# Kernel tuning notes

Measured on AMD Instinct MI355X. Metric: run time of the kernel, lower is better.

## Reference

```python
import jax, jax.numpy as jnp
import numpy as np

NUM_GRAPHS = 128

def gcn_conv(x, edge_index, W, b):
    # PyG GCNConv: add self-loops, sym-normalize, aggregate.
    n = x.shape[0]
    src, dst = edge_index[0], edge_index[1]
    h = x @ W                                   # [N, H]
    deg = jnp.zeros((n,), h.dtype).at[dst].add(1.0) + 1.0  # +1 for self-loop
    dinv = jax.lax.rsqrt(deg)                   # deg^-1/2
    norm = dinv[src] * dinv[dst]                # [E]
    msg = h[src] * norm[:, None]                # [E, H] gathered messages
    agg = jnp.zeros_like(h).at[dst].add(msg)    # scatter-add to dst
    agg = agg + h * (dinv * dinv)[:, None]      # self-loop term
    return agg + b


def setup_inputs() -> dict:
    key = jax.random.key(0)
    ks = jax.random.split(key, 12)
    N, E, F, H, C = 50000, 800000, 64, 64, 16
    x = jax.random.normal(ks[0], (N, F), jnp.float32)
    edge_index = jax.random.randint(ks[1], (2, E), 0, N, jnp.int64)
    batch = jnp.sort(jax.random.randint(ks[2], (N,), 0, NUM_GRAPHS, jnp.int64))
    s = lambda k, sh: jax.random.normal(k, sh, jnp.float32) * (1.0 / np.sqrt(sh[0]))
    return {
        "x": x, "edge_index": edge_index, "batch": batch,
        "W1": s(ks[3], (F, H)), "b1": jnp.zeros((H,), jnp.float32),
        "W2": s(ks[4], (H, H)), "b2": jnp.zeros((H,), jnp.float32),
        "Wc1": s(ks[5], (H, H)), "bc1": jnp.zeros((H,), jnp.float32),
        "Wc2": s(ks[6], (H, C)), "bc2": jnp.zeros((C,), jnp.float32),
    }


def reference(x, edge_index, batch, W1, b1, W2, b2, Wc1, bc1, Wc2, bc2):
    h = gcn_conv(x, edge_index, W1, b1)
    h = jax.nn.relu(h)
    # F.dropout(p=0.5, training=self.training): identity in eval mode
    h = gcn_conv(h, edge_index, W2, b2)
    # global mean pool over graphs
    sums = jax.ops.segment_sum(h, batch, num_segments=NUM_GRAPHS)
    cnts = jax.ops.segment_sum(jnp.ones((h.shape[0],), h.dtype), batch,
                               num_segments=NUM_GRAPHS)
    graph_reps = sums / jnp.maximum(cnts, 1.0)[:, None]
    logits = jax.nn.relu(graph_reps @ Wc1 + bc1) @ Wc2 + bc2
    return (h, graph_reps, logits)
```

## Files before the change

### kernel.cpp

```cpp
#include <hip/hip_runtime.h>
#include <hip/hip_bf16.h>

typedef __hip_bfloat16 bf16;

#define NGRAPH 128
#define MAXNB 256
#define BCAP 8192

__global__ __launch_bounds__(256) void bucket_count_kernel(const int* __restrict__ ei,
                                                           int* __restrict__ bucket_cnt,
                                                           int E, int N, int nb) {
    __shared__ int hist[MAXNB];
    for (int i = threadIdx.x; i < nb; i += 256) hist[i] = 0;
    __syncthreads();
    int stride = gridDim.x * 256;
    for (int e = blockIdx.x * 256 + threadIdx.x; e < E; e += stride) {
        int d = ei[E + e];
        d = max(0, min(d, N - 1));
        atomicAdd(&hist[d >> 8], 1);
    }
    __syncthreads();
    for (int i = threadIdx.x; i < nb; i += 256) {
        int c = hist[i];
        if (c) atomicAdd(&bucket_cnt[i], c);
    }
}

__global__ __launch_bounds__(256) void bucket_scan_kernel(const int* __restrict__ bucket_cnt,
                                                          int* __restrict__ bucket_off,
                                                          int* __restrict__ bucket_cur, int nb) {
    __shared__ int tmp[256];
    int tid = threadIdx.x;
    int v = (tid < nb) ? bucket_cnt[tid] : 0;
    tmp[tid] = v;
    __syncthreads();
    for (int off = 1; off < 256; off <<= 1) {
        int t = (tid >= off) ? tmp[tid - off] : 0;
        __syncthreads();
        tmp[tid] += t;
        __syncthreads();
    }
    int excl = tmp[tid] - v;
    if (tid < nb) { bucket_off[tid] = excl; bucket_cur[tid] = excl; }
    if (tid == nb - 1) bucket_off[nb] = excl + v;
}

__global__ __launch_bounds__(256) void bucket_scatter_kernel(const int* __restrict__ ei,
                                                             int* __restrict__ bucket_cur,
                                                             int2* __restrict__ pairbuf,
                                                             int E, int N, int nb) {
    __shared__ int hist[MAXNB];
    int nwg = gridDim.x;
    int chunk = (E + nwg - 1) / nwg;
    int e0 = blockIdx.x * chunk;
    int e1 = e0 + chunk; if (e1 > E) e1 = E;
    if (e0 >= e1) return;
    for (int i = threadIdx.x; i < nb; i += 256) hist[i] = 0;
    __syncthreads();
    for (int e = e0 + threadIdx.x; e < e1; e += 256) {
        int d = ei[E + e];
        d = max(0, min(d, N - 1));
        atomicAdd(&hist[d >> 8], 1);
    }
    __syncthreads();
    for (int i = threadIdx.x; i < nb; i += 256) {
        int c = hist[i];
        hist[i] = c ? atomicAdd(&bucket_cur[i], c) : 0;
    }
    __syncthreads();
    for (int e = e0 + threadIdx.x; e < e1; e += 256) {
        int s = ei[e];     s = max(0, min(s, N - 1));
        int d = ei[E + e]; d = max(0, min(d, N - 1));
        int pos = atomicAdd(&hist[d >> 8], 1);
        pairbuf[pos] = make_int2(s, d);
    }
}

__global__ __launch_bounds__(256) void bucket_build_kernel(const int2* __restrict__ pairbuf,
                                                           const int* __restrict__ bucket_off,
                                                           int* __restrict__ row_start,
                                                           float* __restrict__ dinv,
                                                           int* __restrict__ csr_src,
                                                           int E, int N, int nb) {
    __shared__ int deg_l[256];
    __shared__ int cur_l[256];
    __shared__ int stage[BCAP];
    int b = blockIdx.x;
    int node0 = b << 8;
    int nn = N - node0; if (nn > 256) nn = 256;
    int p0 = bucket_off[b], p1 = bucket_off[b + 1];
    int ne = p1 - p0;
    int tid = threadIdx.x;
    deg_l[tid] = 0;
    __syncthreads();
    for (int i = p0 + tid; i < p1; i += 256) {
        int d = pairbuf[i].y;
        atomicAdd(&deg_l[d - node0], 1);
    }
    __syncthreads();
    int v = deg_l[tid];
    for (int off = 1; off < 256; off <<= 1) {
        int t = (tid >= off) ? deg_l[tid - off] : 0;
        __syncthreads();
        deg_l[tid] += t;
        __syncthreads();
    }
    int excl = deg_l[tid] - v;
    if (tid < nn) {
        row_start[node0 + tid] = p0 + excl;
        dinv[node0 + tid] = rsqrtf((float)(v + 1));
    }
    if (b == nb - 1 && tid == nn - 1) row_start[N] = p0 + excl + v;
    cur_l[tid] = excl;
    __syncthreads();
    if (ne <= BCAP) {
        for (int i = p0 + tid; i < p1; i += 256) {
            int2 pr = pairbuf[i];
            int pos = atomicAdd(&cur_l[pr.y - node0], 1);
            stage[pos] = pr.x;
        }
        __syncthreads();
        for (int i = tid; i < ne; i += 256) csr_src[p0 + i] = stage[i];
    } else {
        for (int i = p0 + tid; i < p1; i += 256) {
            int2 pr = pairbuf[i];
            int pos = atomicAdd(&cur_l[pr.y - node0], 1);
            csr_src[p0 + pos] = pr.x;
        }
    }
}

__global__ __launch_bounds__(256) void proj_kernel(const float* __restrict__ A,
                                                   const float* __restrict__ W,
                                                   const float* __restrict__ dinv,
                                                   bf16* __restrict__ P, int N) {
    __shared__ float Wl[4096];
    for (int i = threadIdx.x; i < 4096; i += 256) Wl[i] = W[i];
    __syncthreads();
    int lane = threadIdx.x & 63;
    int wid = (blockIdx.x * 256 + threadIdx.x) >> 6;
    int nwaves = (gridDim.x * 256) >> 6;
    for (int node = wid; node < N; node += nwaves) {
        float a = A[(size_t)node * 64 + lane];
        float acc = 0.f;
#pragma unroll
        for (int k = 0; k < 64; ++k) acc += __shfl(a, k) * Wl[k * 64 + lane];
        P[(size_t)node * 64 + lane] = __float2bfloat16(acc * dinv[node]);
    }
}

__device__ __forceinline__ void acc_bf8(float* acc, uint4 v, float w) {
    unsigned int u[4] = {v.x, v.y, v.z, v.w};
#pragma unroll
    for (int m = 0; m < 4; ++m) {
        float lo = __uint_as_float(u[m] << 16);
        float hi = __uint_as_float(u[m] & 0xffff0000u);
        acc[2 * m]     += w * lo;
        acc[2 * m + 1] += w * hi;
    }
}

__device__ __forceinline__ void gather_sum8(float* acc,
                                            const bf16* __restrict__ P,
                                            const int* __restrict__ csr_src,
                                            int beg, int end, int r, int c) {
#pragma unroll
    for (int k = 0; k < 8; ++k) acc[k] = 0.f;
    for (int i = beg; i < end; i += 16) {
        int r0 = i + r, r1 = i + 8 + r;
        int ok0 = (r0 < end), ok1 = (r1 < end);
        int s0 = ok0 ? csr_src[r0] : 0;
        int s1 = ok1 ? csr_src[r1] : 0;
        float w0 = ok0 ? 1.f : 0.f;
        float w1 = ok1 ? 1.f : 0.f;
        uint4 v0 = *(const uint4*)(P + (size_t)s0 * 64 + c * 8);
        uint4 v1 = *(const uint4*)(P + (size_t)s1 * 64 + c * 8);
        acc_bf8(acc, v0, w0);
        acc_bf8(acc, v1, w1);
    }
#pragma unroll
    for (int mask = 8; mask <= 32; mask <<= 1) {
#pragma unroll
        for (int k = 0; k < 8; ++k) acc[k] += __shfl_xor(acc[k], mask);
    }
}

__global__ __launch_bounds__(256) void agg_proj_kernel(const bf16* __restrict__ P1,
                                                       const int* __restrict__ row_start,
                                                       const int* __restrict__ csr_src,
                                                       const float* __restrict__ dinv,
                                                       const float* __restrict__ b1,
                                                       const float* __restrict__ W2,
                                                       bf16* __restrict__ P2, int N) {
    __shared__ float Wl[4096];
    for (int i = threadIdx.x; i < 4096; i += 256) Wl[i] = W2[i];
    __syncthreads();
    int lane = threadIdx.x & 63;
    int r = lane >> 3, c = lane & 7;
    float bb[8];
#pragma unroll
    for (int k = 0; k < 8; ++k) bb[k] = b1[c * 8 + k];
    int wid = (blockIdx.x * 256 + threadIdx.x) >> 6;
    int nwaves = (gridDim.x * 256) >> 6;
    int cpn = (N + nwaves - 1) / nwaves;
    int node0 = wid * cpn;
    int node1 = node0 + cpn; if (node1 > N) node1 = N;
    for (int node = node0; node < node1; ++node) {
        float acc[8];
        gather_sum8(acc, P1, csr_src, row_start[node], row_start[node + 1], r, c);
        uint4 vs = *(const uint4*)(P1 + (size_t)node * 64 + c * 8);
        acc_bf8(acc, vs, 1.f);
        float dv = dinv[node];
        float h[8];
#pragma unroll
        for (int k = 0; k < 8; ++k) h[k] = fmaxf(acc[k] * dv + bb[k], 0.f);
        float acc2 = 0.f;
#pragma unroll
        for (int c2 = 0; c2 < 8; ++c2) {
#pragma unroll
            for (int j = 0; j < 8; ++j) {
                acc2 += __shfl(h[j], c2) * Wl[(c2 * 8 + j) * 64 + lane];
            }
        }
        P2[(size_t)node * 64 + lane] = __float2bfloat16(acc2 * dv);
    }
}

__global__ __launch_bounds__(256) void agg_pool_kernel(const bf16* __restrict__ P2,
                                                       const int* __restrict__ row_start,
                                                       const int* __restrict__ csr_src,
                                                       const float* __restrict__ dinv,
                                                       const float* __restrict__ b2,
                                                       const int* __restrict__ batch,
                                                       float* __restrict__ out_h,
                                                       float* __restrict__ accum, int N) {
    int lane = threadIdx.x & 63;
    int r = lane >> 3, c = lane & 7;
    float bb[8];
#pragma unroll
    for (int k = 0; k < 8; ++k) bb[k] = b2[c * 8 + k];
    int src = ((lane & 7) << 3) | (lane >> 3);
    int wid = (blockIdx.x * 256 + threadIdx.x) >> 6;
    int nwaves = (gridDim.x * 256) >> 6;
    int cpn = (N + nwaves - 1) / nwaves;
    int node0 = wid * cpn;
    int node1 = node0 + cpn; if (node1 > N) node1 = N;
    for (int node = node0; node < node1; ++node) {
        float acc[8];
        gather_sum8(acc, P2, csr_src, row_start[node], row_start[node + 1], r, c);
        uint4 vs = *(const uint4*)(P2 + (size_t)node * 64 + c * 8);
        acc_bf8(acc, vs, 1.f);
        float dv = dinv[node];
        float h[8];
#pragma unroll
        for (int k = 0; k < 8; ++k) h[k] = acc[k] * dv + bb[k];
        float val = 0.f;
#pragma unroll
        for (int k = 0; k < 8; ++k) {
            float t = __shfl(h[k], src);
            val = ((lane & 7) == k) ? t : val;
        }
        out_h[(size_t)node * 64 + lane] = val;
        int g = batch[node];
        g = max(0, min(g, NGRAPH - 1));
        atomicAdd(&accum[g * 64 + lane], val);
    }
}

__device__ __forceinline__ int lower_bound_dev(const int* a, int n, int key) {
    int lo = 0, hi = n;
    while (lo < hi) {
        int mid = (lo + hi) >> 1;
        if (a[mid] < key) lo = mid + 1; else hi = mid;
    }
    return lo;
}

__global__ __launch_bounds__(64) void final_kernel(const float* __restrict__ accum,
                                                   const int* __restrict__ batch,
                                                   const float* __restrict__ Wc1,
                                                   const float* __restrict__ bc1,
                                                   const float* __restrict__ Wc2,
                                                   const float* __restrict__ bc2,
                                                   float* __restrict__ out_reps,
                                                   float* __restrict__ out_logits, int N) {
    __shared__ float rep[64];
    __shared__ float t[64];
    int g = blockIdx.x;
    int f = threadIdx.x;
    int lo = lower_bound_dev(batch, N, g);
    int hi = lower_bound_dev(batch, N, g + 1);
    float cnt = (float)(hi - lo);
    float r = accum[g * 64 + f] / fmaxf(cnt, 1.f);
    out_reps[g * 64 + f] = r;
    rep[f] = r;
    __syncthreads();
    float acc = bc1[f];
#pragma unroll
    for (int k = 0; k < 64; ++k) acc += rep[k] * Wc1[k * 64 + f];
    t[f] = fmaxf(acc, 0.f);
    __syncthreads();
    if (f < 16) {
        float a2 = bc2[f];
#pragma unroll
        for (int k = 0; k < 64; ++k) a2 += t[k] * Wc2[k * 16 + f];
        out_logits[g * 16 + f] = a2;
    }
}

extern "C" void kernel_launch(void* const* d_in, const int* in_sizes, int n_in,
                              void* d_out, int out_size, void* d_ws, size_t ws_size,
                              hipStream_t stream) {
    const float* x    = (const float*)d_in[0];
    const int*   ei   = (const int*)d_in[1];
    const int*   batch= (const int*)d_in[2];
    const float* W1   = (const float*)d_in[3];
    const float* b1   = (const float*)d_in[4];
    const float* W2   = (const float*)d_in[5];
    const float* b2   = (const float*)d_in[6];
    const float* Wc1  = (const float*)d_in[7];
    const float* bc1  = (const float*)d_in[8];
    const float* Wc2  = (const float*)d_in[9];
    const float* bc2  = (const float*)d_in[10];

    const int N = in_sizes[2];
    const int E = in_sizes[1] / 2;
    const int nb = (N + 255) >> 8;

    char* ws = (char*)d_ws;
    size_t off = 0;
    auto alloc = [&](size_t bytes) { void* p = ws + off; off += (bytes + 255) & ~(size_t)255; return p; };
    float* accum      = (float*)alloc((size_t)NGRAPH * 64 * 4);
    int*   bucket_cnt = (int*)  alloc((size_t)MAXNB * 4);
    size_t zero_bytes = off;
    int*   bucket_off = (int*)  alloc((size_t)(MAXNB + 1) * 4);
    int*   bucket_cur = (int*)  alloc((size_t)MAXNB * 4);
    float* dinv       = (float*)alloc((size_t)N * 4);
    int*   row_start  = (int*)  alloc((size_t)(N + 1) * 4);
    int*   csr_src    = (int*)  alloc((size_t)E * 4);
    bf16*  P1         = (bf16*) alloc((size_t)N * 64 * 2);
    size_t p2_bytes   = (size_t)N * 64 * 2;
    size_t pair_bytes = (size_t)E * 8;
    void*  p2_region  = alloc(p2_bytes > pair_bytes ? p2_bytes : pair_bytes);
    bf16*  P2         = (bf16*)p2_region;
    int2*  pairbuf    = (int2*)p2_region;
    (void)ws_size; (void)n_in; (void)out_size;

    float* out_h      = (float*)d_out;
    float* out_reps   = out_h + (size_t)N * 64;
    float* out_logits = out_reps + (size_t)NGRAPH * 64;

    const int GS = 2048;

    hipMemsetAsync(d_ws, 0, zero_bytes, stream);
    bucket_count_kernel<<<256, 256, 0, stream>>>(ei, bucket_cnt, E, N, nb);
    bucket_scan_kernel<<<1, 256, 0, stream>>>(bucket_cnt, bucket_off, bucket_cur, nb);
    bucket_scatter_kernel<<<256, 256, 0, stream>>>(ei, bucket_cur, pairbuf, E, N, nb);
    bucket_build_kernel<<<nb, 256, 0, stream>>>(pairbuf, bucket_off, row_start, dinv,
                                                csr_src, E, N, nb);

    proj_kernel<<<GS, 256, 0, stream>>>(x, W1, dinv, P1, N);
    agg_proj_kernel<<<GS, 256, 0, stream>>>(P1, row_start, csr_src, dinv, b1, W2, P2, N);
    agg_pool_kernel<<<GS, 256, 0, stream>>>(P2, row_start, csr_src, dinv, b2, batch,
                                            out_h, accum, N);
    final_kernel<<<NGRAPH, 64, 0, stream>>>(accum, batch, Wc1, bc1, Wc2, bc2,
                                            out_reps, out_logits, N);
}
```

Before: 254.8 us.

## Process two nodes per wavefront using half-wave gathers in aggregation kernels

Each 64-lane wavefront now splits into two 32-lane halves, and each half aggregates a different node. Nodes are assigned to waves with a grid stride over node pairs instead of contiguous chunks. With an average degree of about 16, the old 16-row gather left many lanes idle on short rows. Half-waves cut that waste and shorten the shuffle reduction, at the cost of more shuffles per output in the projection and pooling steps. The projection now does 64 shuffles to produce two outputs per lane, and the pooling step issues two atomics per lane.

```diff
diff --git a/kernel.cpp b/kernel.cpp
--- a/kernel.cpp
+++ b/kernel.cpp
@@ -160,14 +160,14 @@
     }
 }
 
-__device__ __forceinline__ void gather_sum8(float* acc,
+__device__ __forceinline__ void gather_half(float acc[8],
                                             const bf16* __restrict__ P,
                                             const int* __restrict__ csr_src,
                                             int beg, int end, int r, int c) {
 #pragma unroll
     for (int k = 0; k < 8; ++k) acc[k] = 0.f;
-    for (int i = beg; i < end; i += 16) {
-        int r0 = i + r, r1 = i + 8 + r;
+    for (int i = beg; i < end; i += 8) {
+        int r0 = i + r, r1 = i + 4 + r;
         int ok0 = (r0 < end), ok1 = (r1 < end);
         int s0 = ok0 ? csr_src[r0] : 0;
         int s1 = ok1 ? csr_src[r1] : 0;
@@ -179,7 +179,7 @@
         acc_bf8(acc, v1, w1);
     }
 #pragma unroll
-    for (int mask = 8; mask <= 32; mask <<= 1) {
+    for (int mask = 8; mask <= 16; mask <<= 1) {
 #pragma unroll
         for (int k = 0; k < 8; ++k) acc[k] += __shfl_xor(acc[k], mask);
     }
@@ -196,33 +196,40 @@
     for (int i = threadIdx.x; i < 4096; i += 256) Wl[i] = W2[i];
     __syncthreads();
     int lane = threadIdx.x & 63;
-    int r = lane >> 3, c = lane & 7;
+    int half = lane >> 5;
+    int hl = lane & 31;
+    int r = hl >> 3, c = hl & 7;
     float bb[8];
 #pragma unroll
     for (int k = 0; k < 8; ++k) bb[k] = b1[c * 8 + k];
     int wid = (blockIdx.x * 256 + threadIdx.x) >> 6;
     int nwaves = (gridDim.x * 256) >> 6;
-    int cpn = (N + nwaves - 1) / nwaves;
-    int node0 = wid * cpn;
-    int node1 = node0 + cpn; if (node1 > N) node1 = N;
-    for (int node = node0; node < node1; ++node) {
+    int npairs = (N + 1) >> 1;
+    for (int p = wid; p < npairs; p += nwaves) {
+        int node = 2 * p + half;
+        int ok = node < N;
+        int nd = ok ? node : N - 1;
+        int beg = row_start[nd];
+        int end = ok ? row_start[nd + 1] : beg;
         float acc[8];
-        gather_sum8(acc, P1, csr_src, row_start[node], row_start[node + 1], r, c);
-        uint4 vs = *(const uint4*)(P1 + (size_t)node * 64 + c * 8);
+        gather_half(acc, P1, csr_src, beg, end, r, c);
+        uint4 vs = *(const uint4*)(P1 + (size_t)nd * 64 + c * 8);
         acc_bf8(acc, vs, 1.f);
-        float dv = dinv[node];
+        float dv = dinv[nd];
         float h[8];
 #pragma unroll
         for (int k = 0; k < 8; ++k) h[k] = fmaxf(acc[k] * dv + bb[k], 0.f);
-        float acc2 = 0.f;
-#pragma unroll
-        for (int c2 = 0; c2 < 8; ++c2) {
-#pragma unroll
-            for (int j = 0; j < 8; ++j) {
-                acc2 += __shfl(h[j], c2) * Wl[(c2 * 8 + j) * 64 + lane];
-            }
-        }
-        P2[(size_t)node * 64 + lane] = __float2bfloat16(acc2 * dv);
+        float a2lo = 0.f, a2hi = 0.f;
+#pragma unroll
+        for (int j = 0; j < 64; ++j) {
+            float hj = __shfl(h[j & 7], (j >> 3) + (half << 5));
+            a2lo += hj * Wl[j * 64 + hl];
+            a2hi += hj * Wl[j * 64 + hl + 32];
+        }
+        if (ok) {
+            P2[(size_t)node * 64 + hl]      = __float2bfloat16(a2lo * dv);
+            P2[(size_t)node * 64 + hl + 32] = __float2bfloat16(a2hi * dv);
+        }
     }
 }
 
@@ -235,35 +242,46 @@
                                                        float* __restrict__ out_h,
                                                        float* __restrict__ accum, int N) {
     int lane = threadIdx.x & 63;
-    int r = lane >> 3, c = lane & 7;
+    int half = lane >> 5;
+    int hl = lane & 31;
+    int r = hl >> 3, c = hl & 7;
     float bb[8];
 #pragma unroll
     for (int k = 0; k < 8; ++k) bb[k] = b2[c * 8 + k];
-    int src = ((lane & 7) << 3) | (lane >> 3);
+    int src_lo = (hl >> 3) + (half << 5);
+    int src_hi = (hl >> 3) + 4 + (half << 5);
     int wid = (blockIdx.x * 256 + threadIdx.x) >> 6;
     int nwaves = (gridDim.x * 256) >> 6;
-    int cpn = (N + nwaves - 1) / nwaves;
-    int node0 = wid * cpn;
-    int node1 = node0 + cpn; if (node1 > N) node1 = N;
-    for (int node = node0; node < node1; ++node) {
+    int npairs = (N + 1) >> 1;
+    for (int p = wid; p < npairs; p += nwaves) {
+        int node = 2 * p + half;
+        int ok = node < N;
+        int nd = ok ? node : N - 1;
+        int beg = row_start[nd];
+        int end = ok ? row_start[nd + 1] : beg;
         float acc[8];
-        gather_sum8(acc, P2, csr_src, row_start[node], row_start[node + 1], r, c);
-        uint4 vs = *(const uint4*)(P2 + (size_t)node * 64 + c * 8);
+        gather_half(acc, P2, csr_src, beg, end, r, c);
+        uint4 vs = *(const uint4*)(P2 + (size_t)nd * 64 + c * 8);
         acc_bf8(acc, vs, 1.f);
-        float dv = dinv[node];
+        float dv = dinv[nd];
         float h[8];
 #pragma unroll
         for (int k = 0; k < 8; ++k) h[k] = acc[k] * dv + bb[k];
-        float val = 0.f;
+        float vlo = 0.f, vhi = 0.f;
 #pragma unroll
         for (int k = 0; k < 8; ++k) {
-            float t = __shfl(h[k], src);
-            val = ((lane & 7) == k) ? t : val;
-        }
-        out_h[(size_t)node * 64 + lane] = val;
-        int g = batch[node];
-        g = max(0, min(g, NGRAPH - 1));
-        atomicAdd(&accum[g * 64 + lane], val);
+            float tlo = __shfl(h[k], src_lo);
+            float thi = __shfl(h[k], src_hi);
+            if ((hl & 7) == k) { vlo = tlo; vhi = thi; }
+        }
+        if (ok) {
+            out_h[(size_t)node * 64 + hl]      = vlo;
+            out_h[(size_t)node * 64 + hl + 32] = vhi;
+            int g = batch[nd];
+            g = max(0, min(g, NGRAPH - 1));
+            atomicAdd(&accum[g * 64 + hl], vlo);
+            atomicAdd(&accum[g * 64 + hl + 32], vhi);
+        }
     }
 }
 
```

Result: slower. 310.7 us (+21.9%).
